# Optimization experiments

Measured on AMD Instinct MI355X. Metric: run time of the kernel, lower is better.

## Reference

```python
import jax, jax.numpy as jnp
import numpy as np

N, F_IN, H, C = 100000, 256, 128, 64
E, EP = 1600000, 500000


def setup_inputs() -> dict:
    key = jax.random.key(0)
    ks = jax.random.split(key, 8)
    x = jax.random.normal(ks[0], (N, F_IN), jnp.float32)
    masked_nodes = jax.random.randint(ks[1], (1000,), 0, N)
    pos_edge_index = jax.random.randint(ks[2], (2, EP), 0, N)
    neg_edge_index = jax.random.randint(ks[3], (2, EP), 0, N)
    edge_index = jax.random.randint(ks[4], (2, E), 0, N)
    W1 = jax.random.normal(ks[5], (F_IN, H), jnp.float32) / np.sqrt(F_IN).astype(np.float32)
    b1 = jnp.zeros((H,), jnp.float32)
    W2 = jax.random.normal(ks[6], (H, C), jnp.float32) / np.sqrt(H).astype(np.float32)
    b2 = jnp.zeros((C,), jnp.float32)
    return dict(x=x, masked_nodes=masked_nodes, pos_edge_index=pos_edge_index,
                neg_edge_index=neg_edge_index, edge_index=edge_index,
                W1=W1, b1=b1, W2=W2, b2=b2)


def gcn_conv(x, W, b, src, dst, n):
    # PyG GCNConv: h = x @ W; symmetric norm with self-loops; aggregate; + bias
    h = x @ W  # [N, out]
    deg = jax.ops.segment_sum(jnp.ones(src.shape[0], h.dtype), dst, num_segments=n) + 1.0
    dis = jax.lax.rsqrt(deg)  # D^{-1/2} including self-loop
    msg = h[src] * (dis[src] * dis[dst])[:, None]           # gather + edge-norm
    agg = jax.ops.segment_sum(msg, dst, num_segments=n)      # scatter-add
    agg = agg + h * (dis * dis)[:, None]                      # self-loop term
    return agg + b


def reference(x, masked_nodes, pos_edge_index, neg_edge_index, edge_index, W1, b1, W2, b2):
    n = x.shape[0]
    src, dst = edge_index[0], edge_index[1]
    h = jax.nn.relu(gcn_conv(x, W1, b1, src, dst, n))
    h = gcn_conv(h, W2, b2, src, dst, n)  # [N, C]
    tei = jnp.concatenate([pos_edge_index, neg_edge_index], axis=-1)  # [2, 2*EP]
    x_j = h[tei[0]]  # [2EP, C]
    x_i = h[tei[1]]
    scores = jnp.einsum('ef,ef->e', x_i, x_j)
    return scores, jnp.zeros(tei.shape, jnp.float32)
```

## Files before the change

kernel.cpp:

```cpp
#include <hip/hip_runtime.h>

#define N_NODES 100000
#define F_IN    256
#define H_DIM   128
#define C_DIM   64
#define E_EDGES 1600000
#define EP_EDGES 500000

#define NBUK 391
#define EPB  4096

typedef unsigned short bf16_t;
typedef short  short8  __attribute__((ext_vector_type(8)));
typedef float  float4v __attribute__((ext_vector_type(4)));

__device__ inline bf16_t f2bf(float f) {
    unsigned u = __float_as_uint(f);
    u += 0x7fff + ((u >> 16) & 1);
    return (bf16_t)(u >> 16);
}
__device__ inline float bf2f(bf16_t h) {
    return __uint_as_float(((unsigned)h) << 16);
}
__device__ inline void split8(const float* vv, short* h, short* l) {
#pragma unroll
    for (int j = 0; j < 8; ++j) {
        bf16_t hb = f2bf(vv[j]);
        h[j] = (short)hb;
        l[j] = (short)f2bf(vv[j] - bf2f(hb));
    }
}
__device__ inline float4v mfma16(short8 a, short8 b, float4v c) {
    return __builtin_amdgcn_mfma_f32_16x16x32_bf16(a, b, c, 0, 0, 0);
}

__global__ __launch_bounds__(256) void bhist_kernel(const int* __restrict__ dst,
                                                    int* __restrict__ bsize) {
    __shared__ int hist[NBUK];
    const int t = threadIdx.x;
    for (int b = t; b < NBUK; b += 256) hist[b] = 0;
    __syncthreads();
    const int e0 = blockIdx.x * EPB;
#pragma unroll
    for (int i = 0; i < 16; ++i) {
        int e = e0 + i * 256 + t;
        if (e < E_EDGES) atomicAdd(&hist[dst[e] >> 8], 1);
    }
    __syncthreads();
    for (int b = t; b < NBUK; b += 256)
        if (hist[b]) atomicAdd(&bsize[b], hist[b]);
}

__global__ __launch_bounds__(512) void bscan_kernel(const int* __restrict__ bsize,
                                                    int* __restrict__ bbase,
                                                    int* __restrict__ bcursor) {
    __shared__ int sh[512];
    int t = threadIdx.x;
    sh[t] = (t < NBUK) ? bsize[t] : 0;
    __syncthreads();
#pragma unroll
    for (int off = 1; off < 512; off <<= 1) {
        int u = (t >= off) ? sh[t - off] : 0;
        __syncthreads();
        sh[t] += u;
        __syncthreads();
    }
    if (t < NBUK) {
        int ex = (t == 0) ? 0 : sh[t - 1];
        bbase[t] = ex;
        bcursor[t] = ex;
    }
    if (t == 0) bbase[NBUK] = E_EDGES;
}

__global__ __launch_bounds__(256) void bucket_scatter_kernel(const int* __restrict__ src,
                                                             const int* __restrict__ dst,
                                                             int* __restrict__ bcursor,
                                                             int2* __restrict__ pairs) {
    __shared__ int hist[NBUK];
    __shared__ int base[NBUK];
    const int t = threadIdx.x;
    for (int b = t; b < NBUK; b += 256) hist[b] = 0;
    __syncthreads();

    const int e0 = blockIdx.x * EPB;
    int s[16], d[16];
#pragma unroll
    for (int i = 0; i < 16; ++i) {
        int e = e0 + i * 256 + t;
        if (e < E_EDGES) {
            s[i] = src[e];
            d[i] = dst[e];
            atomicAdd(&hist[d[i] >> 8], 1);
        } else {
            d[i] = -1;
        }
    }
    __syncthreads();
    for (int b = t; b < NBUK; b += 256) {
        int c = hist[b];
        base[b] = c ? atomicAdd(&bcursor[b], c) : 0;
        hist[b] = 0;
    }
    __syncthreads();
#pragma unroll
    for (int i = 0; i < 16; ++i) {
        if (d[i] >= 0) {
            int b = d[i] >> 8;
            int r = atomicAdd(&hist[b], 1);
            pairs[base[b] + r] = make_int2(s[i], d[i]);
        }
    }
}

__global__ __launch_bounds__(256) void bucket_sort_kernel(const int2* __restrict__ pairs,
                                                          const int* __restrict__ bbase,
                                                          int* __restrict__ row_ptr,
                                                          float* __restrict__ dis,
                                                          int* __restrict__ csr_src) {
    __shared__ int cnt[256];
    __shared__ int sh[256];
    __shared__ int cur[256];
    const int b = blockIdx.x;
    const int node0 = b << 8;
    const int t = threadIdx.x;
    const int nn = min(256, N_NODES - node0);
    const int beg = bbase[b], end = bbase[b + 1];
    cnt[t] = 0;
    __syncthreads();
    for (int e = beg + t; e < end; e += 256)
        atomicAdd(&cnt[pairs[e].y - node0], 1);
    __syncthreads();
    int c = cnt[t];
    if (t < nn) dis[node0 + t] = rsqrtf((float)c + 1.0f);
    sh[t] = c;
    __syncthreads();
#pragma unroll
    for (int off = 1; off < 256; off <<= 1) {
        int u = (t >= off) ? sh[t - off] : 0;
        __syncthreads();
        sh[t] += u;
        __syncthreads();
    }
    int start = beg + sh[t] - c;
    if (t < nn) row_ptr[node0 + t] = start;
    cur[t] = start;
    if (b == NBUK - 1 && t == 0) row_ptr[N_NODES] = E_EDGES;
    __syncthreads();
    for (int e = beg + t; e < end; e += 256) {
        int2 p = pairs[e];
        int j = atomicAdd(&cur[p.y - node0], 1);
        csr_src[j] = p.x;
    }
}

__global__ __launch_bounds__(256) void wprep_kernel(const float* __restrict__ W1,
                                                    const float* __restrict__ W2,
                                                    short* __restrict__ w1h,
                                                    short* __restrict__ w1l,
                                                    short* __restrict__ w2h,
                                                    short* __restrict__ w2l) {
    int idx = blockIdx.x * 256 + threadIdx.x;
    if (idx < H_DIM * F_IN) {
        int n = idx >> 8, k = idx & 255;
        float w = W1[k * H_DIM + n];
        bf16_t h = f2bf(w);
        w1h[idx] = (short)h;
        w1l[idx] = (short)f2bf(w - bf2f(h));
    }
    int i2 = idx - H_DIM * F_IN;
    if (i2 >= 0 && i2 < C_DIM * H_DIM) {
        int n = i2 >> 7, k = i2 & 127;
        float w = W2[k * C_DIM + n];
        bf16_t h = f2bf(w);
        w2h[i2] = (short)h;
        w2l[i2] = (short)f2bf(w - bf2f(h));
    }
}

#define LSTR 40
__global__ __launch_bounds__(256) void gemm1_mfma(const float* __restrict__ X,
                                                  const short* __restrict__ Wth,
                                                  const short* __restrict__ Wtl,
                                                  bf16_t* __restrict__ T,
                                                  int nrows) {
    __shared__ short Ah[128 * LSTR], Al[128 * LSTR];
    __shared__ short Bh[128 * LSTR], Bl[128 * LSTR];
    const int t = threadIdx.x;
    const int row0 = blockIdx.x * 128;
    const int w = t >> 6;
    const int lane = t & 63;
    const int m = lane & 15;
    const int q = lane >> 4;
    const int koff = q * 8;

    float4v acc[2][8];
#pragma unroll
    for (int i = 0; i < 2; ++i)
#pragma unroll
        for (int j = 0; j < 8; ++j) acc[i][j] = {0.f, 0.f, 0.f, 0.f};

    for (int ks = 0; ks < 8; ++ks) {
        const int k0 = ks * 32;
#pragma unroll
        for (int i = 0; i < 2; ++i) {
            int c = t + i * 256;
            int r = c >> 2, kc = c & 3;
            int row = row0 + r;
            float vv[8] = {0.f, 0.f, 0.f, 0.f, 0.f, 0.f, 0.f, 0.f};
            if (row < nrows) {
                float4 v0 = *(const float4*)&X[(long long)row * F_IN + k0 + kc * 8];
                float4 v1 = *(const float4*)&X[(long long)row * F_IN + k0 + kc * 8 + 4];
                vv[0] = v0.x; vv[1] = v0.y; vv[2] = v0.z; vv[3] = v0.w;
                vv[4] = v1.x; vv[5] = v1.y; vv[6] = v1.z; vv[7] = v1.w;
            }
            short h[8], l[8];
            split8(vv, h, l);
            *(short8*)&Ah[r * LSTR + kc * 8] = *(short8*)h;
            *(short8*)&Al[r * LSTR + kc * 8] = *(short8*)l;
        }
#pragma unroll
        for (int i = 0; i < 2; ++i) {
            int c = t + i * 256;
            int n = c >> 2, kc = c & 3;
            *(short8*)&Bh[n * LSTR + kc * 8] = *(const short8*)&Wth[n * F_IN + k0 + kc * 8];
            *(short8*)&Bl[n * LSTR + kc * 8] = *(const short8*)&Wtl[n * F_IN + k0 + kc * 8];
        }
        __syncthreads();

        short8 ah0 = *(const short8*)&Ah[(w * 32 + m) * LSTR + koff];
        short8 ah1 = *(const short8*)&Ah[(w * 32 + 16 + m) * LSTR + koff];
        short8 al0 = *(const short8*)&Al[(w * 32 + m) * LSTR + koff];
        short8 al1 = *(const short8*)&Al[(w * 32 + 16 + m) * LSTR + koff];
#pragma unroll
        for (int nc = 0; nc < 8; ++nc) {
            short8 bh = *(const short8*)&Bh[(nc * 16 + m) * LSTR + koff];
            short8 bl = *(const short8*)&Bl[(nc * 16 + m) * LSTR + koff];
            acc[0][nc] = mfma16(ah0, bh, acc[0][nc]);
            acc[0][nc] = mfma16(al0, bh, acc[0][nc]);
            acc[0][nc] = mfma16(ah0, bl, acc[0][nc]);
            acc[1][nc] = mfma16(ah1, bh, acc[1][nc]);
            acc[1][nc] = mfma16(al1, bh, acc[1][nc]);
            acc[1][nc] = mfma16(ah1, bl, acc[1][nc]);
        }
        __syncthreads();
    }
#pragma unroll
    for (int mt = 0; mt < 2; ++mt)
#pragma unroll
        for (int nc = 0; nc < 8; ++nc)
#pragma unroll
            for (int reg = 0; reg < 4; ++reg) {
                int grow = row0 + w * 32 + mt * 16 + q * 4 + reg;
                int gcol = nc * 16 + m;
                if (grow < nrows)
                    T[(long long)grow * H_DIM + gcol] = f2bf(acc[mt][nc][reg]);
            }
}

__global__ __launch_bounds__(256) void gemm2_mfma(const float* __restrict__ A,
                                                  const float* __restrict__ b1,
                                                  const short* __restrict__ Wth,
                                                  const short* __restrict__ Wtl,
                                                  bf16_t* __restrict__ T,
                                                  int nrows) {
    __shared__ short Ah[128 * LSTR], Al[128 * LSTR];
    __shared__ short Bh[64 * LSTR], Bl[64 * LSTR];
    const int t = threadIdx.x;
    const int row0 = blockIdx.x * 128;
    const int w = t >> 6;
    const int lane = t & 63;
    const int m = lane & 15;
    const int q = lane >> 4;
    const int koff = q * 8;

    float4v acc[2][4];
#pragma unroll
    for (int i = 0; i < 2; ++i)
#pragma unroll
        for (int j = 0; j < 4; ++j) acc[i][j] = {0.f, 0.f, 0.f, 0.f};

    for (int ks = 0; ks < 4; ++ks) {
        const int k0 = ks * 32;
#pragma unroll
        for (int i = 0; i < 2; ++i) {
            int c = t + i * 256;
            int r = c >> 2, kc = c & 3;
            int row = row0 + r;
            float vv[8] = {0.f, 0.f, 0.f, 0.f, 0.f, 0.f, 0.f, 0.f};
            if (row < nrows) {
                float4 v0 = *(const float4*)&A[(long long)row * H_DIM + k0 + kc * 8];
                float4 v1 = *(const float4*)&A[(long long)row * H_DIM + k0 + kc * 8 + 4];
                float4 b0 = *(const float4*)&b1[k0 + kc * 8];
                float4 b1v = *(const float4*)&b1[k0 + kc * 8 + 4];
                vv[0] = fmaxf(v0.x + b0.x, 0.f);  vv[1] = fmaxf(v0.y + b0.y, 0.f);
                vv[2] = fmaxf(v0.z + b0.z, 0.f);  vv[3] = fmaxf(v0.w + b0.w, 0.f);
                vv[4] = fmaxf(v1.x + b1v.x, 0.f); vv[5] = fmaxf(v1.y + b1v.y, 0.f);
                vv[6] = fmaxf(v1.z + b1v.z, 0.f); vv[7] = fmaxf(v1.w + b1v.w, 0.f);
            }
            short h[8], l[8];
            split8(vv, h, l);
            *(short8*)&Ah[r * LSTR + kc * 8] = *(short8*)h;
            *(short8*)&Al[r * LSTR + kc * 8] = *(short8*)l;
        }
        {
            int n = t >> 2, kc = t & 3;
            *(short8*)&Bh[n * LSTR + kc * 8] = *(const short8*)&Wth[n * H_DIM + k0 + kc * 8];
            *(short8*)&Bl[n * LSTR + kc * 8] = *(const short8*)&Wtl[n * H_DIM + k0 + kc * 8];
        }
        __syncthreads();

        short8 ah0 = *(const short8*)&Ah[(w * 32 + m) * LSTR + koff];
        short8 ah1 = *(const short8*)&Ah[(w * 32 + 16 + m) * LSTR + koff];
        short8 al0 = *(const short8*)&Al[(w * 32 + m) * LSTR + koff];
        short8 al1 = *(const short8*)&Al[(w * 32 + 16 + m) * LSTR + koff];
#pragma unroll
        for (int nc = 0; nc < 4; ++nc) {
            short8 bh = *(const short8*)&Bh[(nc * 16 + m) * LSTR + koff];
            short8 bl = *(const short8*)&Bl[(nc * 16 + m) * LSTR + koff];
            acc[0][nc] = mfma16(ah0, bh, acc[0][nc]);
            acc[0][nc] = mfma16(al0, bh, acc[0][nc]);
            acc[0][nc] = mfma16(ah0, bl, acc[0][nc]);
            acc[1][nc] = mfma16(ah1, bh, acc[1][nc]);
            acc[1][nc] = mfma16(al1, bh, acc[1][nc]);
            acc[1][nc] = mfma16(ah1, bl, acc[1][nc]);
        }
        __syncthreads();
    }
#pragma unroll
    for (int mt = 0; mt < 2; ++mt)
#pragma unroll
        for (int nc = 0; nc < 4; ++nc)
#pragma unroll
            for (int reg = 0; reg < 4; ++reg) {
                int grow = row0 + w * 32 + mt * 16 + q * 4 + reg;
                int gcol = nc * 16 + m;
                if (grow < nrows)
                    T[(long long)grow * C_DIM + gcol] = f2bf(acc[mt][nc][reg]);
            }
}

__device__ inline void fma8_bf16(float* acc, uint4 u, float c) {
#pragma unroll
    for (int p = 0; p < 4; ++p) {
        unsigned w = (&u.x)[p];
        float lo = __uint_as_float(w << 16);
        float hi = __uint_as_float(w & 0xffff0000u);
        acc[2 * p]     = fmaf(lo, c, acc[2 * p]);
        acc[2 * p + 1] = fmaf(hi, c, acc[2 * p + 1]);
    }
}

template <int CS, bool HAS_BIAS>
__global__ __launch_bounds__(256) void agg_kernel(const bf16_t* __restrict__ t,
                                                  const float* __restrict__ dis,
                                                  const int* __restrict__ row_ptr,
                                                  const int* __restrict__ csr_src,
                                                  const float* __restrict__ bias,
                                                  float* __restrict__ agg) {
    unsigned idx = blockIdx.x * 256u + threadIdx.x;
    if (idx >= (unsigned)(N_NODES << CS)) return;
    int node = idx >> CS;
    int q = idx & ((1 << CS) - 1);
    const uint4* tv = (const uint4*)t;
    float dd = dis[node];
    int beg = row_ptr[node], end = row_ptr[node + 1];

    float acc[8];
#pragma unroll
    for (int p = 0; p < 8; ++p) acc[p] = 0.0f;
    fma8_bf16(acc, tv[idx], dd * dd);

    int j = beg;
    for (; j + 3 < end; j += 4) {
        int s0 = csr_src[j + 0], s1 = csr_src[j + 1];
        int s2 = csr_src[j + 2], s3 = csr_src[j + 3];
        float c0 = dis[s0] * dd, c1 = dis[s1] * dd;
        float c2 = dis[s2] * dd, c3 = dis[s3] * dd;
        uint4 u0 = tv[((unsigned)s0 << CS) + q];
        uint4 u1 = tv[((unsigned)s1 << CS) + q];
        uint4 u2 = tv[((unsigned)s2 << CS) + q];
        uint4 u3 = tv[((unsigned)s3 << CS) + q];
        fma8_bf16(acc, u0, c0);
        fma8_bf16(acc, u1, c1);
        fma8_bf16(acc, u2, c2);
        fma8_bf16(acc, u3, c3);
    }
    for (; j < end; ++j) {
        int s = csr_src[j];
        float c = dis[s] * dd;
        fma8_bf16(acc, tv[((unsigned)s << CS) + q], c);
    }

    if (HAS_BIAS) {
        float4 bv0 = ((const float4*)bias)[q * 2];
        float4 bv1 = ((const float4*)bias)[q * 2 + 1];
        acc[0] += bv0.x; acc[1] += bv0.y; acc[2] += bv0.z; acc[3] += bv0.w;
        acc[4] += bv1.x; acc[5] += bv1.y; acc[6] += bv1.z; acc[7] += bv1.w;
    }
    float4 o0 = make_float4(acc[0], acc[1], acc[2], acc[3]);
    float4 o1 = make_float4(acc[4], acc[5], acc[6], acc[7]);
    ((float4*)agg)[idx * 2]     = o0;
    ((float4*)agg)[idx * 2 + 1] = o1;
}

__global__ __launch_bounds__(256) void score_kernel(const float* __restrict__ h2,
                                                    const int* __restrict__ pos,
                                                    const int* __restrict__ neg,
                                                    float* __restrict__ out) {
    int tid = blockIdx.x * 256 + threadIdx.x;
    int e = tid >> 4;
    int q = tid & 15;
    if (e >= 2 * EP_EDGES) return;
    int i, j;
    if (e < EP_EDGES) {
        j = pos[e];
        i = pos[EP_EDGES + e];
    } else {
        j = neg[e - EP_EDGES];
        i = neg[e];
    }
    float4 a = ((const float4*)h2)[i * (C_DIM / 4) + q];
    float4 b = ((const float4*)h2)[j * (C_DIM / 4) + q];
    float v = a.x * b.x + a.y * b.y + a.z * b.z + a.w * b.w;
    v += __shfl_down(v, 8, 16);
    v += __shfl_down(v, 4, 16);
    v += __shfl_down(v, 2, 16);
    v += __shfl_down(v, 1, 16);
    if (q == 0) out[e] = v;
}

extern "C" void kernel_launch(void* const* d_in, const int* in_sizes, int n_in,
                              void* d_out, int out_size, void* d_ws, size_t ws_size,
                              hipStream_t stream) {
    const float* x  = (const float*)d_in[0];
    const int* pos  = (const int*)d_in[2];
    const int* neg  = (const int*)d_in[3];
    const int* ei   = (const int*)d_in[4];
    const float* W1 = (const float*)d_in[5];
    const float* b1 = (const float*)d_in[6];
    const float* W2 = (const float*)d_in[7];
    const float* b2 = (const float*)d_in[8];
    float* out = (float*)d_out;

    char* ws = (char*)d_ws;
    float*  dis     = (float*) (ws + 0);
    int*    row_ptr = (int*)   (ws + 400000);
    int*    bsize   = (int*)   (ws + 800128);
    int*    bbase   = (int*)   (ws + 801792);
    int*    bcursor = (int*)   (ws + 803456);
    int*    csr_src = (int*)   (ws + 805120);
    int2*   pairs   = (int2*)  (ws + 7205120);
    bf16_t* t       = (bf16_t*)(ws + 20005120);
    float*  agg     = (float*) (ws + 45605120);
    short*  w1th    = (short*) (ws + 96805120);
    short*  w1tl    = (short*) (ws + 96870656);
    short*  w2th    = (short*) (ws + 96936192);
    short*  w2tl    = (short*) (ws + 96952576);

    const int* esrc = ei;
    const int* edst = ei + E_EDGES;

    hipMemsetAsync(bsize, 0, NBUK * sizeof(int), stream);
    bhist_kernel<<<(E_EDGES + EPB - 1) / EPB, 256, 0, stream>>>(edst, bsize);
    bscan_kernel<<<1, 512, 0, stream>>>(bsize, bbase, bcursor);
    bucket_scatter_kernel<<<(E_EDGES + EPB - 1) / EPB, 256, 0, stream>>>(
        esrc, edst, bcursor, pairs);
    bucket_sort_kernel<<<NBUK, 256, 0, stream>>>(pairs, bbase, row_ptr, dis, csr_src);
    wprep_kernel<<<(H_DIM * F_IN + C_DIM * H_DIM + 255) / 256, 256, 0, stream>>>(
        W1, W2, w1th, w1tl, w2th, w2tl);

    gemm1_mfma<<<(N_NODES + 127) / 128, 256, 0, stream>>>(x, w1th, w1tl, t, N_NODES);
    agg_kernel<4, false><<<(N_NODES * 16 + 255) / 256, 256, 0, stream>>>(
        t, dis, row_ptr, csr_src, nullptr, agg);

    gemm2_mfma<<<(N_NODES + 127) / 128, 256, 0, stream>>>(agg, b1, w2th, w2tl, t, N_NODES);
    agg_kernel<3, true><<<(N_NODES * 8 + 255) / 256, 256, 0, stream>>>(
        t, dis, row_ptr, csr_src, b2, agg);

    score_kernel<<<(2 * EP_EDGES * 16) / 256, 256, 0, stream>>>(agg, pos, neg, out);

    hipMemsetAsync(out + 2 * EP_EDGES, 0, (size_t)4 * EP_EDGES * sizeof(float), stream);
}
```

Baseline: 438.6 us.

## Load MFMA operands directly from global memory, dropping LDS staging in both GEMMs

Both dense GEMM kernels now have each lane load its A-row fragment and B-weight fragment straight from global memory into registers in MFMA layout. This removes the shared-memory tiles and both __syncthreads per K-step. The goal is to cut LDS traffic and barrier stalls and to let loads from consecutive K-steps overlap. In exchange, the weight fragments are re-read from global/L2 by every wave instead of being shared through LDS, and the X reads become strided per lane rather than fully coalesced.

After: 481.8 us. 9.8% more time.

```diff
diff --git a/kernel.cpp b/kernel.cpp
--- a/kernel.cpp
+++ b/kernel.cpp
@@ -178,21 +178,26 @@
     }
 }
 
-#define LSTR 40
 __global__ __launch_bounds__(256) void gemm1_mfma(const float* __restrict__ X,
                                                   const short* __restrict__ Wth,
                                                   const short* __restrict__ Wtl,
                                                   bf16_t* __restrict__ T,
                                                   int nrows) {
-    __shared__ short Ah[128 * LSTR], Al[128 * LSTR];
-    __shared__ short Bh[128 * LSTR], Bl[128 * LSTR];
     const int t = threadIdx.x;
     const int row0 = blockIdx.x * 128;
     const int w = t >> 6;
     const int lane = t & 63;
     const int m = lane & 15;
     const int q = lane >> 4;
-    const int koff = q * 8;
+
+    const int r0 = row0 + w * 32 + m;
+    const int r1 = r0 + 16;
+    const bool ok0 = r0 < nrows;
+    const bool ok1 = r1 < nrows;
+    const float* X0 = X + (long long)r0 * F_IN + q * 8;
+    const float* X1 = X + (long long)r1 * F_IN + q * 8;
+    const short* Bh0 = Wth + m * F_IN + q * 8;
+    const short* Bl0 = Wtl + m * F_IN + q * 8;
 
     float4v acc[2][8];
 #pragma unroll
@@ -200,42 +205,26 @@
 #pragma unroll
         for (int j = 0; j < 8; ++j) acc[i][j] = {0.f, 0.f, 0.f, 0.f};
 
+#pragma unroll 2
     for (int ks = 0; ks < 8; ++ks) {
         const int k0 = ks * 32;
-#pragma unroll
-        for (int i = 0; i < 2; ++i) {
-            int c = t + i * 256;
-            int r = c >> 2, kc = c & 3;
-            int row = row0 + r;
-            float vv[8] = {0.f, 0.f, 0.f, 0.f, 0.f, 0.f, 0.f, 0.f};
-            if (row < nrows) {
-                float4 v0 = *(const float4*)&X[(long long)row * F_IN + k0 + kc * 8];
-                float4 v1 = *(const float4*)&X[(long long)row * F_IN + k0 + kc * 8 + 4];
-                vv[0] = v0.x; vv[1] = v0.y; vv[2] = v0.z; vv[3] = v0.w;
-                vv[4] = v1.x; vv[5] = v1.y; vv[6] = v1.z; vv[7] = v1.w;
-            }
-            short h[8], l[8];
-            split8(vv, h, l);
-            *(short8*)&Ah[r * LSTR + kc * 8] = *(short8*)h;
-            *(short8*)&Al[r * LSTR + kc * 8] = *(short8*)l;
-        }
-#pragma unroll
-        for (int i = 0; i < 2; ++i) {
-            int c = t + i * 256;
-            int n = c >> 2, kc = c & 3;
-            *(short8*)&Bh[n * LSTR + kc * 8] = *(const short8*)&Wth[n * F_IN + k0 + kc * 8];
-            *(short8*)&Bl[n * LSTR + kc * 8] = *(const short8*)&Wtl[n * F_IN + k0 + kc * 8];
-        }
-        __syncthreads();
-
-        short8 ah0 = *(const short8*)&Ah[(w * 32 + m) * LSTR + koff];
-        short8 ah1 = *(const short8*)&Ah[(w * 32 + 16 + m) * LSTR + koff];
-        short8 al0 = *(const short8*)&Al[(w * 32 + m) * LSTR + koff];
-        short8 al1 = *(const short8*)&Al[(w * 32 + 16 + m) * LSTR + koff];
+        float a0[8] = {0.f, 0.f, 0.f, 0.f, 0.f, 0.f, 0.f, 0.f};
+        float a1[8] = {0.f, 0.f, 0.f, 0.f, 0.f, 0.f, 0.f, 0.f};
+        if (ok0) {
+            *(float4*)&a0[0] = *(const float4*)&X0[k0];
+            *(float4*)&a0[4] = *(const float4*)&X0[k0 + 4];
+        }
+        if (ok1) {
+            *(float4*)&a1[0] = *(const float4*)&X1[k0];
+            *(float4*)&a1[4] = *(const float4*)&X1[k0 + 4];
+        }
+        short8 ah0, al0, ah1, al1;
+        split8(a0, (short*)&ah0, (short*)&al0);
+        split8(a1, (short*)&ah1, (short*)&al1);
 #pragma unroll
         for (int nc = 0; nc < 8; ++nc) {
-            short8 bh = *(const short8*)&Bh[(nc * 16 + m) * LSTR + koff];
-            short8 bl = *(const short8*)&Bl[(nc * 16 + m) * LSTR + koff];
+            short8 bh = *(const short8*)&Bh0[nc * 16 * F_IN + k0];
+            short8 bl = *(const short8*)&Bl0[nc * 16 * F_IN + k0];
             acc[0][nc] = mfma16(ah0, bh, acc[0][nc]);
             acc[0][nc] = mfma16(al0, bh, acc[0][nc]);
             acc[0][nc] = mfma16(ah0, bl, acc[0][nc]);
@@ -243,7 +232,6 @@
             acc[1][nc] = mfma16(al1, bh, acc[1][nc]);
             acc[1][nc] = mfma16(ah1, bl, acc[1][nc]);
         }
-        __syncthreads();
     }
 #pragma unroll
     for (int mt = 0; mt < 2; ++mt)
@@ -264,15 +252,22 @@
                                                   const short* __restrict__ Wtl,
                                                   bf16_t* __restrict__ T,
                                                   int nrows) {
-    __shared__ short Ah[128 * LSTR], Al[128 * LSTR];
-    __shared__ short Bh[64 * LSTR], Bl[64 * LSTR];
     const int t = threadIdx.x;
     const int row0 = blockIdx.x * 128;
     const int w = t >> 6;
     const int lane = t & 63;
     const int m = lane & 15;
     const int q = lane >> 4;
-    const int koff = q * 8;
+
+    const int r0 = row0 + w * 32 + m;
+    const int r1 = r0 + 16;
+    const bool ok0 = r0 < nrows;
+    const bool ok1 = r1 < nrows;
+    const float* A0 = A + (long long)r0 * H_DIM + q * 8;
+    const float* A1 = A + (long long)r1 * H_DIM + q * 8;
+    const float* bp = b1 + q * 8;
+    const short* Bh0 = Wth + m * H_DIM + q * 8;
+    const short* Bl0 = Wtl + m * H_DIM + q * 8;
 
     float4v acc[2][4];
 #pragma unroll
@@ -280,44 +275,36 @@
 #pragma unroll
         for (int j = 0; j < 4; ++j) acc[i][j] = {0.f, 0.f, 0.f, 0.f};
 
+#pragma unroll 2
     for (int ks = 0; ks < 4; ++ks) {
         const int k0 = ks * 32;
-#pragma unroll
-        for (int i = 0; i < 2; ++i) {
-            int c = t + i * 256;
-            int r = c >> 2, kc = c & 3;
-            int row = row0 + r;
-            float vv[8] = {0.f, 0.f, 0.f, 0.f, 0.f, 0.f, 0.f, 0.f};
-            if (row < nrows) {
-                float4 v0 = *(const float4*)&A[(long long)row * H_DIM + k0 + kc * 8];
-                float4 v1 = *(const float4*)&A[(long long)row * H_DIM + k0 + kc * 8 + 4];
-                float4 b0 = *(const float4*)&b1[k0 + kc * 8];
-                float4 b1v = *(const float4*)&b1[k0 + kc * 8 + 4];
-                vv[0] = fmaxf(v0.x + b0.x, 0.f);  vv[1] = fmaxf(v0.y + b0.y, 0.f);
-                vv[2] = fmaxf(v0.z + b0.z, 0.f);  vv[3] = fmaxf(v0.w + b0.w, 0.f);
-                vv[4] = fmaxf(v1.x + b1v.x, 0.f); vv[5] = fmaxf(v1.y + b1v.y, 0.f);
-                vv[6] = fmaxf(v1.z + b1v.z, 0.f); vv[7] = fmaxf(v1.w + b1v.w, 0.f);
-            }
-            short h[8], l[8];
-            split8(vv, h, l);
-            *(short8*)&Ah[r * LSTR + kc * 8] = *(short8*)h;
-            *(short8*)&Al[r * LSTR + kc * 8] = *(short8*)l;
-        }
-        {
-            int n = t >> 2, kc = t & 3;
-            *(short8*)&Bh[n * LSTR + kc * 8] = *(const short8*)&Wth[n * H_DIM + k0 + kc * 8];
-            *(short8*)&Bl[n * LSTR + kc * 8] = *(const short8*)&Wtl[n * H_DIM + k0 + kc * 8];
-        }
-        __syncthreads();
-
-        short8 ah0 = *(const short8*)&Ah[(w * 32 + m) * LSTR + koff];
-        short8 ah1 = *(const short8*)&Ah[(w * 32 + 16 + m) * LSTR + koff];
-        short8 al0 = *(const short8*)&Al[(w * 32 + m) * LSTR + koff];
-        short8 al1 = *(const short8*)&Al[(w * 32 + 16 + m) * LSTR + koff];
+        float4 bv0 = *(const float4*)&bp[k0];
+        float4 bv1 = *(const float4*)&bp[k0 + 4];
+        float a0[8] = {0.f, 0.f, 0.f, 0.f, 0.f, 0.f, 0.f, 0.f};
+        float a1[8] = {0.f, 0.f, 0.f, 0.f, 0.f, 0.f, 0.f, 0.f};
+        if (ok0) {
+            float4 v0 = *(const float4*)&A0[k0];
+            float4 v1 = *(const float4*)&A0[k0 + 4];
+            a0[0] = fmaxf(v0.x + bv0.x, 0.f); a0[1] = fmaxf(v0.y + bv0.y, 0.f);
+            a0[2] = fmaxf(v0.z + bv0.z, 0.f); a0[3] = fmaxf(v0.w + bv0.w, 0.f);
+            a0[4] = fmaxf(v1.x + bv1.x, 0.f); a0[5] = fmaxf(v1.y + bv1.y, 0.f);
+            a0[6] = fmaxf(v1.z + bv1.z, 0.f); a0[7] = fmaxf(v1.w + bv1.w, 0.f);
+        }
+        if (ok1) {
+            float4 v0 = *(const float4*)&A1[k0];
+            float4 v1 = *(const float4*)&A1[k0 + 4];
+            a1[0] = fmaxf(v0.x + bv0.x, 0.f); a1[1] = fmaxf(v0.y + bv0.y, 0.f);
+            a1[2] = fmaxf(v0.z + bv0.z, 0.f); a1[3] = fmaxf(v0.w + bv0.w, 0.f);
+            a1[4] = fmaxf(v1.x + bv1.x, 0.f); a1[5] = fmaxf(v1.y + bv1.y, 0.f);
+            a1[6] = fmaxf(v1.z + bv1.z, 0.f); a1[7] = fmaxf(v1.w + bv1.w, 0.f);
+        }
+        short8 ah0, al0, ah1, al1;
+        split8(a0, (short*)&ah0, (short*)&al0);
+        split8(a1, (short*)&ah1, (short*)&al1);
 #pragma unroll
         for (int nc = 0; nc < 4; ++nc) {
-            short8 bh = *(const short8*)&Bh[(nc * 16 + m) * LSTR + koff];
-            short8 bl = *(const short8*)&Bl[(nc * 16 + m) * LSTR + koff];
+            short8 bh = *(const short8*)&Bh0[nc * 16 * H_DIM + k0];
+            short8 bl = *(const short8*)&Bl0[nc * 16 * H_DIM + k0];
             acc[0][nc] = mfma16(ah0, bh, acc[0][nc]);
             acc[0][nc] = mfma16(al0, bh, acc[0][nc]);
             acc[0][nc] = mfma16(ah0, bl, acc[0][nc]);
@@ -325,7 +312,6 @@
             acc[1][nc] = mfma16(al1, bh, acc[1][nc]);
             acc[1][nc] = mfma16(ah1, bl, acc[1][nc]);
         }
-        __syncthreads();
     }
 #pragma unroll
     for (int mt = 0; mt < 2; ++mt)
```
